# Performance work log

Hardware: AMD Instinct MI355X
Metric: run time of the kernel (lower is better)

## Reference

```python
import jax, jax.numpy as jnp
import numpy as np

BITS = 4
GROUP_SIZE = 128
IN_FEATURES = 4096
OUT_FEATURES = 14336
M = 256  # rows of x; >= kernel_switch_threshold so torch takes the dequant+matmul path


def setup_inputs() -> dict:
    key = jax.random.key(0)
    k1, k2, k3, k4 = jax.random.split(key, 4)
    x = jax.random.normal(k1, (M, IN_FEATURES), dtype=jnp.float16)
    # packed int4 weights: in_features//32*bits rows of int32
    qweight = jax.random.randint(
        k2, (IN_FEATURES // 32 * BITS, OUT_FEATURES), 0, 2**31 - 1, dtype=jnp.int32
    )
    n_groups = IN_FEATURES // GROUP_SIZE
    scales = jax.random.uniform(k3, (n_groups, OUT_FEATURES), dtype=jnp.float32) * 0.01 + 0.001
    # note: module stores zeros as scale*zero product (see pack()); any float works
    zeros = jax.random.uniform(k4, (n_groups, OUT_FEATURES), dtype=jnp.float32) * 0.05
    return {"x": x, "qweight": qweight, "scales": scales, "zeros": zeros}


def reference(x, qweight, scales, zeros):
    # Unpack 8 int4 values from each int32 (little-endian nibbles), matching
    # torch: (qweight[:,None,:] >> wf) & 0xF with wf = [0,4,...,28].
    shifts = jnp.arange(0, 32, BITS, dtype=jnp.int32)          # [8]
    w = (qweight[:, None, :] >> shifts[None, :, None]) & (2**BITS - 1)  # [K/8, 8, N]
    w = w.reshape(-1, GROUP_SIZE, qweight.shape[1])             # [n_groups, group, N]
    s = scales.astype(jnp.float16)[:, None, :]                  # [n_groups, 1, N]
    z = zeros.astype(jnp.float16)[:, None, :]
    # group-wise asymmetric dequant: scale * q - (scale*zero)
    w = (s * w.astype(jnp.float16) - z).reshape(-1, qweight.shape[1])  # [K, N]
    out = jnp.matmul(x, w)                                      # [M, N] fp16
    return out.astype(x.dtype)
```

## Files before the change

### kernel.cpp

```cpp
#include <hip/hip_runtime.h>
#include <hip/hip_fp16.h>

typedef unsigned int u32;
typedef unsigned short u16;
typedef __attribute__((ext_vector_type(8))) _Float16 f16x8;
typedef __attribute__((ext_vector_type(4))) float f32x4;
typedef __attribute__((ext_vector_type(4))) u32 u32x4;

#define K_DIM 4096
#define N_DIM 14336
#define BM 64
#define BN 128
#define BK 128
#define NITER (K_DIM / BK)
#define NBLK 448
#define LDA 136

union U4F8 { u32x4 u; f16x8 v; };

__device__ __forceinline__ f16x8 dq8(u32 q, __half2 s2, __half2 d2, __half2 z2) {
  const u32 q1 = q >> 4, q2 = q >> 8, q3 = q >> 12;
  U4F8 r;
  const u32 x0 = ( q & 0x000F000Fu) | 0x64006400u;
  const u32 x1 = (q1 & 0x000F000Fu) | 0x64006400u;
  const u32 x2 = (q2 & 0x000F000Fu) | 0x64006400u;
  const u32 x3 = (q3 & 0x000F000Fu) | 0x64006400u;
  r.u.x = __builtin_bit_cast(u32, __hsub2(__hfma2(__builtin_bit_cast(__half2, x0), s2, d2), z2));
  r.u.y = __builtin_bit_cast(u32, __hsub2(__hfma2(__builtin_bit_cast(__half2, x1), s2, d2), z2));
  r.u.z = __builtin_bit_cast(u32, __hsub2(__hfma2(__builtin_bit_cast(__half2, x2), s2, d2), z2));
  r.u.w = __builtin_bit_cast(u32, __hsub2(__hfma2(__builtin_bit_cast(__half2, x3), s2, d2), z2));
  return r.v;
}

__device__ __forceinline__ u32 pkrtz(float a, float b) {
  return __builtin_bit_cast(u32, __builtin_amdgcn_cvt_pkrtz(a, b));
}

__global__ __launch_bounds__(512, 4) void kivi_gemm(
    const float* __restrict__ X,
    const int* __restrict__ QW,
    const float* __restrict__ S,
    const float* __restrict__ Z,
    float* __restrict__ O)
{
  __shared__ __align__(16) u16 As[2][BM][LDA];

  const int tid  = threadIdx.x;
  const int lane = tid & 63;
  const int w    = tid >> 6;

  const int b  = blockIdx.x;
  const int L  = (b & 7) * 56 + (b >> 3);
  const int m0 = (L & 3) * BM;
  const int n0 = (L >> 2) * BN;

  const int wm = w >> 2, wn = w & 3;
  const int mb = wm * 32, nb = wn * 32;
  const int fr = lane & 15, fq = lane >> 4;
  const int cb = n0 + nb + fr;

  const int arow = tid >> 3;
  const int acol = (tid & 7) * 16;

  f32x4 acc[2][2];
#pragma unroll
  for (int mi = 0; mi < 2; ++mi)
#pragma unroll
    for (int ni = 0; ni < 2; ++ni)
      acc[mi][ni] = (f32x4){0.f, 0.f, 0.f, 0.f};

  f32x4 aReg[4];
  u32 qC[4][2], qN[4][2];
  float svC[2], zvC[2], svN[2], zvN[2];

  auto loadAx = [&](int t) {
    const float* p = X + (size_t)(m0 + arow) * K_DIM + t * BK + acol;
    aReg[0] = *(const f32x4*)(p);
    aReg[1] = *(const f32x4*)(p + 4);
    aReg[2] = *(const f32x4*)(p + 8);
    aReg[3] = *(const f32x4*)(p + 12);
  };
  auto writeAx = [&](int buf) {
#pragma unroll
    for (int c = 0; c < 2; ++c) {
      u32x4 pk;
      pk.x = pkrtz(aReg[c * 2][0], aReg[c * 2 + 1][0]);
      pk.y = pkrtz(aReg[c * 2][1], aReg[c * 2 + 1][1]);
      pk.z = pkrtz(aReg[c * 2][2], aReg[c * 2 + 1][2]);
      pk.w = pkrtz(aReg[c * 2][3], aReg[c * 2 + 1][3]);
      *(u32x4*)&As[buf][arow][acol + c * 8] = pk;
    }
  };
  auto loadBq = [&](int t, u32 (&q)[4][2], float (&s)[2], float (&z)[2]) {
    const size_t rbase = (size_t)(t * 16 + fq) * N_DIM + cb;
#pragma unroll
    for (int ks = 0; ks < 4; ++ks)
#pragma unroll
      for (int ni = 0; ni < 2; ++ni)
        q[ks][ni] = *(const u32*)(QW + rbase + (size_t)ks * 4 * N_DIM + ni * 16);
#pragma unroll
    for (int ni = 0; ni < 2; ++ni) {
      s[ni] = S[(size_t)t * N_DIM + cb + ni * 16];
      z[ni] = Z[(size_t)t * N_DIM + cb + ni * 16];
    }
  };

  loadAx(0);
  loadBq(0, qC, svC, zvC);
  writeAx(0);
  __syncthreads();

  const __half hneg1024 = __float2half(-1024.f);

  for (int i = 0; i < NITER; ++i) {
    const int cur = i & 1;
    const bool pf = (i + 1 < NITER);

    if (pf) {
      loadAx(i + 1);
      loadBq(i + 1, qN, svN, zvN);
    }

    __half2 s2[2], d2[2], z2[2];
#pragma unroll
    for (int ni = 0; ni < 2; ++ni) {
      const __half sh = __float2half(svC[ni]);
      const __half zh = __float2half(zvC[ni]);
      const __half dh = __hmul(sh, hneg1024);
      s2[ni] = __halves2half2(sh, sh);
      d2[ni] = __halves2half2(dh, dh);
      z2[ni] = __halves2half2(zh, zh);
    }

#pragma unroll
    for (int ks = 0; ks < 4; ++ks) {
      f16x8 af[2], bf[2];
#pragma unroll
      for (int mi = 0; mi < 2; ++mi)
        af[mi] = *(const f16x8*)&As[cur][mb + mi * 16 + fr][ks * 32 + fq * 8];
#pragma unroll
      for (int ni = 0; ni < 2; ++ni)
        bf[ni] = dq8(qC[ks][ni], s2[ni], d2[ni], z2[ni]);
#pragma unroll
      for (int mi = 0; mi < 2; ++mi)
#pragma unroll
        for (int ni = 0; ni < 2; ++ni)
          acc[mi][ni] = __builtin_amdgcn_mfma_f32_16x16x32_f16(
              af[mi], bf[ni], acc[mi][ni], 0, 0, 0);
    }

    if (pf) {
      writeAx(cur ^ 1);
#pragma unroll
      for (int ks = 0; ks < 4; ++ks)
#pragma unroll
        for (int ni = 0; ni < 2; ++ni)
          qC[ks][ni] = qN[ks][ni];
#pragma unroll
      for (int ni = 0; ni < 2; ++ni) {
        svC[ni] = svN[ni]; zvC[ni] = zvN[ni];
      }
    }
    __syncthreads();
  }

#pragma unroll
  for (int mi = 0; mi < 2; ++mi)
#pragma unroll
    for (int ni = 0; ni < 2; ++ni)
#pragma unroll
      for (int r = 0; r < 4; ++r) {
        const int row = m0 + mb + mi * 16 + fq * 4 + r;
        const int col = n0 + nb + ni * 16 + fr;
        O[(size_t)row * N_DIM + col] = acc[mi][ni][r];
      }
}

extern "C" void kernel_launch(void* const* d_in, const int* in_sizes, int n_in,
                              void* d_out, int out_size, void* d_ws, size_t ws_size,
                              hipStream_t stream) {
  const float* X  = (const float*)d_in[0];
  const int*   QW = (const int*)d_in[1];
  const float* S  = (const float*)d_in[2];
  const float* Zp = (const float*)d_in[3];
  float* O = (float*)d_out;
  hipLaunchKernelGGL(kivi_gemm, dim3(NBLK), dim3(512), 0, stream, X, QW, S, Zp, O);
}
```

Baseline: 77.73 us.

## Halve M tile to 4-wave blocks and ping-pong prefetch registers

Block tile height drops from 64 to 32 rows and block size from 512 to 256 threads, so the grid doubles to 896 blocks and the block swizzle is remapped to match. The main loop is manually unrolled by two with alternating register and LDS buffer sets, which removes the per-iteration copy of prefetched weights, scales and zeros. Scheduling barriers keep the global loads ahead of the compute. Per-wave dequant and MFMA work is unchanged; the change aims at finer-grained block scheduling and fewer register moves, at the cost of more blocks each reloading X rows.

```diff
diff --git a/kernel.cpp b/kernel.cpp
--- a/kernel.cpp
+++ b/kernel.cpp
@@ -7,13 +7,14 @@
 typedef __attribute__((ext_vector_type(4))) float f32x4;
 typedef __attribute__((ext_vector_type(4))) u32 u32x4;
 
+#define M_DIM 256
 #define K_DIM 4096
 #define N_DIM 14336
-#define BM 64
+#define BM 32
 #define BN 128
 #define BK 128
 #define NITER (K_DIM / BK)
-#define NBLK 448
+#define NBLK ((M_DIM / BM) * (N_DIM / BN))
 #define LDA 136
 
 union U4F8 { u32x4 u; f16x8 v; };
@@ -36,7 +37,7 @@
   return __builtin_bit_cast(u32, __builtin_amdgcn_cvt_pkrtz(a, b));
 }
 
-__global__ __launch_bounds__(512, 4) void kivi_gemm(
+__global__ __launch_bounds__(256, 4) void kivi_gemm(
     const float* __restrict__ X,
     const int* __restrict__ QW,
     const float* __restrict__ S,
@@ -47,15 +48,14 @@
 
   const int tid  = threadIdx.x;
   const int lane = tid & 63;
-  const int w    = tid >> 6;
+  const int wn   = tid >> 6;
 
   const int b  = blockIdx.x;
-  const int L  = (b & 7) * 56 + (b >> 3);
-  const int m0 = (L & 3) * BM;
-  const int n0 = (L >> 2) * BN;
+  const int L  = (b & 7) * 112 + (b >> 3);
+  const int m0 = (L & 7) * BM;
+  const int n0 = (L >> 3) * BN;
 
-  const int wm = w >> 2, wn = w & 3;
-  const int mb = wm * 32, nb = wn * 32;
+  const int nb = wn * 32;
   const int fr = lane & 15, fq = lane >> 4;
   const int cb = n0 + nb + fr;
 
@@ -69,18 +69,18 @@
     for (int ni = 0; ni < 2; ++ni)
       acc[mi][ni] = (f32x4){0.f, 0.f, 0.f, 0.f};
 
-  f32x4 aReg[4];
-  u32 qC[4][2], qN[4][2];
-  float svC[2], zvC[2], svN[2], zvN[2];
+  f32x4 aR0[4], aR1[4];
+  u32 qS0[4][2], qS1[4][2];
+  float sv0[2], zv0[2], sv1[2], zv1[2];
 
-  auto loadAx = [&](int t) {
+  auto loadAx = [&](int t, f32x4 (&aReg)[4]) {
     const float* p = X + (size_t)(m0 + arow) * K_DIM + t * BK + acol;
     aReg[0] = *(const f32x4*)(p);
     aReg[1] = *(const f32x4*)(p + 4);
     aReg[2] = *(const f32x4*)(p + 8);
     aReg[3] = *(const f32x4*)(p + 12);
   };
-  auto writeAx = [&](int buf) {
+  auto writeAx = [&](int buf, f32x4 (&aReg)[4]) {
 #pragma unroll
     for (int c = 0; c < 2; ++c) {
       u32x4 pk;
@@ -104,43 +104,27 @@
       z[ni] = Z[(size_t)t * N_DIM + cb + ni * 16];
     }
   };
-
-  loadAx(0);
-  loadBq(0, qC, svC, zvC);
-  writeAx(0);
-  __syncthreads();
-
-  const __half hneg1024 = __float2half(-1024.f);
-
-  for (int i = 0; i < NITER; ++i) {
-    const int cur = i & 1;
-    const bool pf = (i + 1 < NITER);
-
-    if (pf) {
-      loadAx(i + 1);
-      loadBq(i + 1, qN, svN, zvN);
-    }
-
+  auto computeT = [&](int buf, u32 (&q)[4][2], float (&s)[2], float (&z)[2]) {
+    const __half hneg1024 = __float2half(-1024.f);
     __half2 s2[2], d2[2], z2[2];
 #pragma unroll
     for (int ni = 0; ni < 2; ++ni) {
-      const __half sh = __float2half(svC[ni]);
-      const __half zh = __float2half(zvC[ni]);
+      const __half sh = __float2half(s[ni]);
+      const __half zh = __float2half(z[ni]);
       const __half dh = __hmul(sh, hneg1024);
       s2[ni] = __halves2half2(sh, sh);
       d2[ni] = __halves2half2(dh, dh);
       z2[ni] = __halves2half2(zh, zh);
     }
-
 #pragma unroll
     for (int ks = 0; ks < 4; ++ks) {
       f16x8 af[2], bf[2];
 #pragma unroll
       for (int mi = 0; mi < 2; ++mi)
-        af[mi] = *(const f16x8*)&As[cur][mb + mi * 16 + fr][ks * 32 + fq * 8];
+        af[mi] = *(const f16x8*)&As[buf][mi * 16 + fr][ks * 32 + fq * 8];
 #pragma unroll
       for (int ni = 0; ni < 2; ++ni)
-        bf[ni] = dq8(qC[ks][ni], s2[ni], d2[ni], z2[ni]);
+        bf[ni] = dq8(q[ks][ni], s2[ni], d2[ni], z2[ni]);
 #pragma unroll
       for (int mi = 0; mi < 2; ++mi)
 #pragma unroll
@@ -148,20 +132,27 @@
           acc[mi][ni] = __builtin_amdgcn_mfma_f32_16x16x32_f16(
               af[mi], bf[ni], acc[mi][ni], 0, 0, 0);
     }
+  };
 
-    if (pf) {
-      writeAx(cur ^ 1);
-#pragma unroll
-      for (int ks = 0; ks < 4; ++ks)
-#pragma unroll
-        for (int ni = 0; ni < 2; ++ni)
-          qC[ks][ni] = qN[ks][ni];
-#pragma unroll
-      for (int ni = 0; ni < 2; ++ni) {
-        svC[ni] = svN[ni]; zvC[ni] = zvN[ni];
-      }
+  loadAx(0, aR0); loadBq(0, qS0, sv0, zv0);
+  writeAx(0, aR0);
+  __syncthreads();
+
+#pragma unroll 1
+  for (int i = 0; i < NITER; i += 2) {
+    if (i + 1 < NITER) { loadAx(i + 1, aR1); loadBq(i + 1, qS1, sv1, zv1); }
+    __builtin_amdgcn_sched_barrier(0);
+    computeT(0, qS0, sv0, zv0);
+    if (i + 1 < NITER) writeAx(1, aR1);
+    __syncthreads();
+
+    if (i + 1 < NITER) {
+      if (i + 2 < NITER) { loadAx(i + 2, aR0); loadBq(i + 2, qS0, sv0, zv0); }
+      __builtin_amdgcn_sched_barrier(0);
+      computeT(1, qS1, sv1, zv1);
+      if (i + 2 < NITER) writeAx(0, aR0);
+      __syncthreads();
     }
-    __syncthreads();
   }
 
 #pragma unroll
@@ -170,7 +161,7 @@
     for (int ni = 0; ni < 2; ++ni)
 #pragma unroll
       for (int r = 0; r < 4; ++r) {
-        const int row = m0 + mb + mi * 16 + fq * 4 + r;
+        const int row = m0 + mi * 16 + fq * 4 + r;
         const int col = n0 + nb + ni * 16 + fr;
         O[(size_t)row * N_DIM + col] = acc[mi][ni][r];
       }
@@ -184,5 +175,5 @@
   const float* S  = (const float*)d_in[2];
   const float* Zp = (const float*)d_in[3];
   float* O = (float*)d_out;
-  hipLaunchKernelGGL(kivi_gemm, dim3(NBLK), dim3(512), 0, stream, X, QW, S, Zp, O);
+  hipLaunchKernelGGL(kivi_gemm, dim3(NBLK), dim3(256), 0, stream, X, QW, S, Zp, O);
 }
```

Result: faster. 69.62 us (-10.4%).
